# Kernel optimization log

Measured on AMD Instinct MI355X. Metric: run time of the kernel, lower is better.

Reference implementation:

```python
import jax, jax.numpy as jnp
import numpy as np

D_MODEL = 768
D_HEAD = 64
BATCH = 2
SEQ = 4096


def setup_inputs() -> dict:
    key = jax.random.key(0)
    k1, k2, k3, k4, k5 = jax.random.split(key, 5)
    x = jax.random.normal(k1, (BATCH, SEQ, D_MODEL), dtype=jnp.float32)
    # causal mask as the module expects: (seq_len, seq_len) float, 1 where attend allowed
    mask = jnp.tril(jnp.ones((SEQ, SEQ), dtype=jnp.float32))
    # weights initialized like the module: randn / sqrt(d_model)
    scale = 1.0 / np.sqrt(D_MODEL)
    Wq = jax.random.normal(k2, (D_HEAD, D_MODEL), dtype=jnp.float32) * scale
    Wk = jax.random.normal(k3, (D_HEAD, D_MODEL), dtype=jnp.float32) * scale
    Wv = jax.random.normal(k4, (D_HEAD, D_MODEL), dtype=jnp.float32) * scale
    Wo = jax.random.normal(k5, (D_MODEL, D_HEAD), dtype=jnp.float32) * scale
    return {"x": x, "mask": mask, "Wq": Wq, "Wk": Wk, "Wv": Wv, "Wo": Wo}


def reference(x, mask, Wq, Wk, Wv, Wo):
    # q,k,v: (B, S, d_head); Linear with weight (out,in) => x @ W.T
    q = jnp.einsum('bsm,hm->bsh', x, Wq)
    k = jnp.einsum('bsm,hm->bsh', x, Wk)
    v = jnp.einsum('bsm,hm->bsh', x, Wv)
    scores = jnp.einsum('bqd,bkd->bqk', q, k) / np.sqrt(D_HEAD)  # (B,S,S)
    seq_len = x.shape[1]
    m = mask[:seq_len, :seq_len]
    # faithful to the torch code: tril(scores) - 1e10 * (1 - mask)
    scores = jnp.tril(scores) - 1e10 * (1.0 - m)
    attn = jax.nn.softmax(scores, axis=-1)
    z = jnp.einsum('bqk,bkd->bqd', attn, v)  # (B,S,d_head)
    out = jnp.einsum('bsh,mh->bsm', z, Wo)   # (B,S,d_model)
    return out
```

## Files before the change

### kernel.cpp

```cpp
#include <hip/hip_runtime.h>
#include <stdint.h>

#define SEQ 4096
#define DM 768
#define DH 64

typedef __attribute__((ext_vector_type(8))) short short8;
typedef __attribute__((ext_vector_type(4))) short short4v;
typedef __attribute__((ext_vector_type(4))) float f32x4;
typedef __attribute__((ext_vector_type(2))) uint32_t uint2v;

#define LOG2E 1.4426950408889634f

static __device__ __forceinline__ short bf16r(float f) {
  union { float f; uint32_t u; } v; v.f = f;
  uint32_t u = v.u;
  return (short)((u + 0x7FFFu + ((u >> 16) & 1u)) >> 16);
}

static __device__ __forceinline__ float bf16f(uint16_t u) {
  union { uint32_t u; float f; } v; v.u = ((uint32_t)u) << 16;
  return v.f;
}

static __device__ __forceinline__ uint32_t cvtpk(float a, float b) {
  uint32_t r;
  asm("v_cvt_pk_bf16_f32 %0, %1, %2" : "=v"(r) : "v"(a), "v"(b));
  return r;
}

static __device__ __forceinline__ int swz(int row, int b) {
  return row * 128 + (b ^ ((row & 7) << 4));
}

__global__ __launch_bounds__(256) void convert_w(
    const float* __restrict__ Wq, const float* __restrict__ Wk,
    const float* __restrict__ Wv, const float* __restrict__ Wo,
    uint16_t* __restrict__ Wb, uint16_t* __restrict__ Wob) {
  int id = blockIdx.x * 256 + threadIdx.x;
  if (id < 36864) {
    int row = id / 192, c4 = id % 192;
    const float* src = (row < 64) ? (Wq + (size_t)row * DM)
                     : (row < 128) ? (Wk + (size_t)(row - 64) * DM)
                                   : (Wv + (size_t)(row - 128) * DM);
    const float sc = (row < 64) ? (0.125f * LOG2E) : 1.0f;
    float4 v = *(const float4*)(src + c4 * 4);
    short4v pk = { bf16r(v.x * sc), bf16r(v.y * sc), bf16r(v.z * sc), bf16r(v.w * sc) };
    *(short4v*)(Wb + (size_t)row * DM + c4 * 4) = pk;
  } else {
    int t = id - 36864;
    int row = t >> 4, c4 = t & 15;
    float4 v = *(const float4*)(Wo + (size_t)row * DH + c4 * 4);
    short4v pk = { bf16r(v.x), bf16r(v.y), bf16r(v.z), bf16r(v.w) };
    *(short4v*)(Wob + (size_t)row * DH + c4 * 4) = pk;
  }
}

__global__ __launch_bounds__(256) void qkv_proj(
    const float* __restrict__ x, const uint16_t* __restrict__ Wb,
    uint16_t* __restrict__ qg, uint16_t* __restrict__ kg, uint16_t* __restrict__ vg) {
  __shared__ char smem[4096 + 24576] __attribute__((aligned(16)));
  char* Xl = smem;
  char* Wl = smem + 4096;
  const int tid = threadIdx.x;
  const int lane = tid & 63, wv = tid >> 6;
  const int l15 = lane & 15, l4 = lane >> 4;
  const int row0 = blockIdx.x * 32;

  const int xr = tid >> 4, xc4 = tid & 15;
  const int wr0 = tid >> 3, wb16 = tid & 7;
  const int mh = wv & 1, ng = wv >> 1;

  f32x4 acc[6];
  #pragma unroll
  for (int j = 0; j < 6; ++j) acc[j] = (f32x4){0.f, 0.f, 0.f, 0.f};

  float4 xreg[2];
  short8 wreg[6];
  xreg[0] = *(const float4*)(x + (size_t)(row0 + xr) * DM + xc4 * 4);
  xreg[1] = *(const float4*)(x + (size_t)(row0 + 16 + xr) * DM + xc4 * 4);
  #pragma unroll
  for (int i = 0; i < 6; ++i)
    wreg[i] = *(const short8*)(Wb + (size_t)(wr0 + i * 32) * DM + wb16 * 8);

  for (int t = 0; t < 12; ++t) {
    __syncthreads();
    {
      short4v p0 = { bf16r(xreg[0].x), bf16r(xreg[0].y), bf16r(xreg[0].z), bf16r(xreg[0].w) };
      *(short4v*)(Xl + swz(xr, xc4 * 8)) = p0;
      short4v p1 = { bf16r(xreg[1].x), bf16r(xreg[1].y), bf16r(xreg[1].z), bf16r(xreg[1].w) };
      *(short4v*)(Xl + swz(xr + 16, xc4 * 8)) = p1;
    }
    #pragma unroll
    for (int i = 0; i < 6; ++i)
      *(short8*)(Wl + swz(wr0 + i * 32, wb16 * 16)) = wreg[i];
    __syncthreads();
    if (t < 11) {
      const int k0n = (t + 1) * 64;
      xreg[0] = *(const float4*)(x + (size_t)(row0 + xr) * DM + k0n + xc4 * 4);
      xreg[1] = *(const float4*)(x + (size_t)(row0 + 16 + xr) * DM + k0n + xc4 * 4);
      #pragma unroll
      for (int i = 0; i < 6; ++i)
        wreg[i] = *(const short8*)(Wb + (size_t)(wr0 + i * 32) * DM + k0n + wb16 * 8);
    }
    #pragma unroll
    for (int kc = 0; kc < 2; ++kc) {
      short8 af = *(const short8*)(Xl + swz(mh * 16 + l15, kc * 64 + l4 * 16));
      #pragma unroll
      for (int j = 0; j < 6; ++j) {
        int nt = ng * 6 + j;
        short8 bfv = *(const short8*)(Wl + swz(nt * 16 + l15, kc * 64 + l4 * 16));
        acc[j] = __builtin_amdgcn_mfma_f32_16x16x32_bf16(af, bfv, acc[j], 0, 0, 0);
      }
    }
  }
  #pragma unroll
  for (int j = 0; j < 6; ++j) {
    int nt = ng * 6 + j;
    uint16_t* dst = (nt < 4) ? qg : (nt < 8) ? kg : vg;
    int cb = (nt & 3) * 16 + l15;
    #pragma unroll
    for (int r = 0; r < 4; ++r) {
      int row = row0 + mh * 16 + l4 * 4 + r;
      dst[(size_t)row * DH + cb] = (uint16_t)bf16r(acc[j][r]);
    }
  }
}

__global__ __launch_bounds__(256) void attn_split(
    const uint16_t* __restrict__ qg, const uint16_t* __restrict__ kg,
    const uint16_t* __restrict__ vg, uint16_t* __restrict__ zg,
    uint16_t* __restrict__ Opart, float* __restrict__ Ml, int CHUNK, int MAXCH) {
  __shared__ char smem[32768 + 4 * 2048] __attribute__((aligned(16)));

  const int tid = threadIdx.x;
  const int lane = tid & 63, wv = tid >> 6;
  const int l15 = lane & 15, l4 = lane >> 4;
  const int qt = blockIdx.x, ch = blockIdx.y, b = blockIdx.z;
  const int q0 = qt << 6;
  const int kv_lim = q0 + 64;
  const int kv_begin = ch * CHUNK;
  if (kv_begin >= kv_lim) return;
  const int kv_end = min(kv_begin + CHUNK, kv_lim);
  const int ntiles = (kv_end - kv_begin) >> 6;

  const uint16_t* qb = qg + (size_t)b * SEQ * DH;
  const uint16_t* kb = kg + (size_t)b * SEQ * DH;
  const uint16_t* vb = vg + (size_t)b * SEQ * DH;

  const int qrow = q0 + wv * 16 + l15;
  short8 qf0 = *(const short8*)(qb + (size_t)qrow * DH + l4 * 8);
  short8 qf1 = *(const short8*)(qb + (size_t)qrow * DH + 32 + l4 * 8);

  int koffA[4], koffB[4], voffA[4], voffB[4];
  #pragma unroll
  for (int n = 0; n < 4; ++n) {
    koffA[n] = swz(n * 16 + l15, l4 * 16);
    koffB[n] = swz(n * 16 + l15, 64 + l4 * 16);
    int dr = n * 16 + l15;
    voffA[n] = 8192 + dr * 128 + ((l4 * 16) ^ ((dr & 7) << 4));
    voffB[n] = 8192 + dr * 128 + ((64 + l4 * 16) ^ ((dr & 7) << 4));
  }
  int pwoff[4];
  #pragma unroll
  for (int n = 0; n < 4; ++n) pwoff[n] = 32768 + wv * 2048 + swz(l15, n * 32 + l4 * 8);
  const int proff0 = 32768 + wv * 2048 + swz(l15, l4 * 16);
  const int proff1 = 32768 + wv * 2048 + swz(l15, 64 + l4 * 16);

  const int ku = tid - 128;
  const int vg_ = tid >> 3, vdg = tid & 7;
  short8 sreg[4];
  int soff[8];
  if (tid >= 128) {
    #pragma unroll
    for (int i = 0; i < 4; ++i) {
      int c = ku + (i << 7);
      soff[i] = swz(c >> 3, (c & 7) * 16);
    }
  } else {
    #pragma unroll
    for (int j = 0; j < 8; ++j) {
      int d = vdg * 8 + j;
      soff[j] = 8192 + d * 128 + ((vg_ * 8) ^ ((d & 7) << 4));
    }
  }

#define LOAD_REGS(KV0)                                                              \
  if (tid >= 128) {                                                                 \
    _Pragma("unroll")                                                               \
    for (int i = 0; i < 4; ++i) {                                                   \
      int c = ku + (i << 7);                                                        \
      sreg[i] = *(const short8*)(kb + (size_t)((KV0) + (c >> 3)) * DH + (c & 7) * 8); \
    }                                                                               \
  } else {                                                                          \
    _Pragma("unroll")                                                               \
    for (int i = 0; i < 4; ++i)                                                     \
      sreg[i] = *(const short8*)(vb + (size_t)((KV0) + vg_ * 4 + i) * DH + vdg * 8); \
  }

#define STAGE_WRITE(BUF)                                                            \
  {                                                                                 \
    char* base_ = smem + ((BUF) << 14);                                             \
    if (tid >= 128) {                                                               \
      _Pragma("unroll")                                                             \
      for (int i = 0; i < 4; ++i) *(short8*)(base_ + soff[i]) = sreg[i];            \
    } else {                                                                        \
      _Pragma("unroll")                                                             \
      for (int j = 0; j < 8; ++j) {                                                 \
        short4v pk = { sreg[0][j], sreg[1][j], sreg[2][j], sreg[3][j] };            \
        *(short4v*)(base_ + soff[j]) = pk;                                          \
      }                                                                             \
    }                                                                               \
  }

  LOAD_REGS(kv_begin);
  STAGE_WRITE(0);

  f32x4 oaccT[4];
  #pragma unroll
  for (int n = 0; n < 4; ++n) oaccT[n] = (f32x4){0.f, 0.f, 0.f, 0.f};
  float lrun = 0.f;

  for (int T = 0; T < ntiles; ++T) {
    const int kv0 = kv_begin + (T << 6);
    const bool more = (T + 1 < ntiles);
    if (more) { LOAD_REGS(kv0 + 64); }
    __syncthreads();
    char* cb_ = smem + ((T & 1) << 14);

    f32x4 sacc[4];
    #pragma unroll
    for (int n = 0; n < 4; ++n) sacc[n] = (f32x4){0.f, 0.f, 0.f, 0.f};
    __builtin_amdgcn_s_setprio(1);
    #pragma unroll
    for (int n = 0; n < 4; ++n) {
      short8 kf0 = *(const short8*)(cb_ + koffA[n]);
      sacc[n] = __builtin_amdgcn_mfma_f32_16x16x32_bf16(kf0, qf0, sacc[n], 0, 0, 0);
      short8 kf1 = *(const short8*)(cb_ + koffB[n]);
      sacc[n] = __builtin_amdgcn_mfma_f32_16x16x32_bf16(kf1, qf1, sacc[n], 0, 0, 0);
    }
    __builtin_amdgcn_s_setprio(0);

    if (more) { STAGE_WRITE((T + 1) & 1); }

    if (kv0 + 63 > q0) {
      #pragma unroll
      for (int n = 0; n < 4; ++n) {
        #pragma unroll
        for (int r = 0; r < 4; ++r) {
          int kvg = kv0 + n * 16 + l4 * 4 + r;
          if (kvg > qrow) sacc[n][r] = -1e30f;
        }
      }
    }

    float ls = 0.f;
    #pragma unroll
    for (int n = 0; n < 4; ++n) {
      #pragma unroll
      for (int r = 0; r < 4; ++r) {
        float p = __builtin_amdgcn_exp2f(sacc[n][r]);
        sacc[n][r] = p;
        ls += p;
      }
    }
    ls += __shfl_xor(ls, 16);
    ls += __shfl_xor(ls, 32);
    lrun += ls;

    #pragma unroll
    for (int n = 0; n < 4; ++n) {
      uint2v pk = { cvtpk(sacc[n][0], sacc[n][1]), cvtpk(sacc[n][2], sacc[n][3]) };
      *(uint2v*)(smem + pwoff[n]) = pk;
    }
    asm volatile("s_waitcnt lgkmcnt(0)" ::: "memory");
    short8 pa0 = *(const short8*)(smem + proff0);
    short8 pa1 = *(const short8*)(smem + proff1);
    __builtin_amdgcn_s_setprio(1);
    #pragma unroll
    for (int n = 0; n < 4; ++n) {
      short8 vf0 = *(const short8*)(cb_ + voffA[n]);
      oaccT[n] = __builtin_amdgcn_mfma_f32_16x16x32_bf16(vf0, pa0, oaccT[n], 0, 0, 0);
      short8 vf1 = *(const short8*)(cb_ + voffB[n]);
      oaccT[n] = __builtin_amdgcn_mfma_f32_16x16x32_bf16(vf1, pa1, oaccT[n], 0, 0, 0);
    }
    __builtin_amdgcn_s_setprio(0);
  }
#undef LOAD_REGS
#undef STAGE_WRITE

  const int rl = wv * 16 + l15;
  if (MAXCH == 1) {
    float invl = 1.0f / lrun;
    uint16_t* zb = zg + (size_t)b * SEQ * DH;
    #pragma unroll
    for (int n = 0; n < 4; ++n) {
      short4v pk = { bf16r(oaccT[n][0] * invl), bf16r(oaccT[n][1] * invl),
                     bf16r(oaccT[n][2] * invl), bf16r(oaccT[n][3] * invl) };
      *(short4v*)(zb + (size_t)(q0 + rl) * DH + n * 16 + l4 * 4) = pk;
    }
  } else {
    const size_t slot = ((size_t)(b << 6) + qt) * MAXCH + ch;
    uint16_t* op = Opart + slot * 4096;
    #pragma unroll
    for (int n = 0; n < 4; ++n) {
      short4v pk = { bf16r(oaccT[n][0]), bf16r(oaccT[n][1]),
                     bf16r(oaccT[n][2]), bf16r(oaccT[n][3]) };
      *(short4v*)(op + (size_t)rl * 64 + n * 16 + l4 * 4) = pk;
    }
    if (l4 == 0) Ml[slot * 64 + rl] = lrun;
  }
}

__global__ __launch_bounds__(256) void out_proj(
    const uint16_t* __restrict__ Opart, const float* __restrict__ Ml,
    const uint16_t* __restrict__ zg, const uint16_t* __restrict__ Wob,
    float* __restrict__ out, int CHUNK, int MAXCH) {
  __shared__ char smem[4096 + 32768] __attribute__((aligned(16)));
  char* Zl = smem;
  char* Wl = smem + 4096;
  const int tid = threadIdx.x;
  const int lane = tid & 63, wv = tid >> 6;
  const int l15 = lane & 15, l4 = lane >> 4;
  const int row0 = blockIdx.x * 32;
  const int col0 = blockIdx.y * 256;

  {
    const int r = tid >> 3, c0 = (tid & 7) << 3;
    if (MAXCH == 1) {
      short8 v = *(const short8*)(zg + (size_t)(row0 + r) * DH + c0);
      *(short8*)(Zl + swz(r, c0 * 2)) = v;
    } else {
      const int b = row0 >> 12;
      const int rlb = row0 & 4095;
      const int qt = rlb >> 6, q0 = qt << 6;
      const int row_local = (rlb & 63) + r;
      const int nch = (q0 + 64 + CHUNK - 1) / CHUNK;
      const size_t sbase = ((size_t)(b << 6) + qt) * MAXCH;
      float a[8] = {0.f, 0.f, 0.f, 0.f, 0.f, 0.f, 0.f, 0.f};
      float wsum = 0.f;
      for (int ch = 0; ch < nch; ++ch) {
        const size_t s = sbase + ch;
        wsum += Ml[s * 64 + row_local];
        short8 v = *(const short8*)(Opart + s * 4096 + (size_t)row_local * 64 + c0);
        #pragma unroll
        for (int j = 0; j < 8; ++j) a[j] += bf16f((uint16_t)v[j]);
      }
      float inv = 1.0f / wsum;
      short8 pk;
      #pragma unroll
      for (int j = 0; j < 8; ++j) pk[j] = bf16r(a[j] * inv);
      *(short8*)(Zl + swz(r, c0 * 2)) = pk;
    }
  }
  #pragma unroll
  for (int i = 0; i < 8; ++i) {
    int id = tid + (i << 8);
    int m = id >> 3, c8 = id & 7;
    short8 vw = *(const short8*)(Wob + (size_t)(col0 + m) * DH + c8 * 8);
    *(short8*)(Wl + swz(m, c8 * 16)) = vw;
  }
  __syncthreads();

  const int mh = wv & 1, ng = wv >> 1;
  short8 af0 = *(const short8*)(Zl + swz(mh * 16 + l15, l4 * 16));
  short8 af1 = *(const short8*)(Zl + swz(mh * 16 + l15, 64 + l4 * 16));
  f32x4 acc[8];
  #pragma unroll
  for (int j = 0; j < 8; ++j) acc[j] = (f32x4){0.f, 0.f, 0.f, 0.f};
  #pragma unroll
  for (int j = 0; j < 8; ++j) {
    int nt = ng * 8 + j;
    short8 b0 = *(const short8*)(Wl + swz(nt * 16 + l15, l4 * 16));
    acc[j] = __builtin_amdgcn_mfma_f32_16x16x32_bf16(af0, b0, acc[j], 0, 0, 0);
    short8 b1 = *(const short8*)(Wl + swz(nt * 16 + l15, 64 + l4 * 16));
    acc[j] = __builtin_amdgcn_mfma_f32_16x16x32_bf16(af1, b1, acc[j], 0, 0, 0);
  }
  #pragma unroll
  for (int j = 0; j < 8; ++j) {
    int nt = ng * 8 + j;
    #pragma unroll
    for (int r = 0; r < 4; ++r) {
      int row = row0 + mh * 16 + l4 * 4 + r;
      int col = col0 + nt * 16 + l15;
      out[(size_t)row * DM + col] = acc[j][r];
    }
  }
}

extern "C" void kernel_launch(void* const* d_in, const int* in_sizes, int n_in,
                              void* d_out, int out_size, void* d_ws, size_t ws_size,
                              hipStream_t stream) {
  const float* x  = (const float*)d_in[0];
  const float* Wq = (const float*)d_in[2];
  const float* Wk = (const float*)d_in[3];
  const float* Wv = (const float*)d_in[4];
  const float* Wo = (const float*)d_in[5];
  float* out = (float*)d_out;

  const size_t N = (size_t)2 * SEQ * DH;
  uint16_t* qg = (uint16_t*)d_ws;
  uint16_t* kg = qg + N;
  uint16_t* vg = kg + N;
  uint16_t* zg = vg + N;
  uint16_t* Wb = zg + N;
  const size_t WBE = (size_t)192 * DM;
  uint16_t* Wob = Wb + WBE;
  const size_t WOE = (size_t)DM * DH;
  uint16_t* Opart = Wob + WOE;

  int maxch = 16;
  while (maxch > 1) {
    size_t slots = (size_t)2 * 64 * maxch;
    size_t need = 4 * N * 2 + WBE * 2 + WOE * 2 + slots * (4096 * 2 + 64 * 4);
    if (need <= ws_size) break;
    maxch >>= 1;
  }
  const int CHUNK = SEQ / maxch;
  float* Ml = (float*)(Opart + (size_t)2 * 64 * maxch * 4096);

  convert_w<<<192, 256, 0, stream>>>(Wq, Wk, Wv, Wo, Wb, Wob);
  qkv_proj<<<256, 256, 0, stream>>>(x, Wb, qg, kg, vg);
  attn_split<<<dim3(64, maxch, 2), 256, 0, stream>>>(qg, kg, vg, zg, Opart, Ml,
                                                     CHUNK, maxch);
  out_proj<<<dim3(256, 3), 256, 0, stream>>>(Opart, Ml, zg, Wob, out, CHUNK, maxch);
}
```

Measured before the change: 51.32 us.

## Load QKV projection operands directly into registers, dropping LDS staging

The QKV projection kernel no longer stages x and weight tiles through shared memory with barriers. Each wave now loads its MFMA fragments straight from global memory and converts x to bf16 with packed cvt instructions, using 16-row blocks of two waves across 512 blocks. This removes the LDS writes, reads and syncthreads, but each wave re-reads weight rows from global memory or cache, and the loads are strided per lane.

```diff
diff --git a/kernel.cpp b/kernel.cpp
--- a/kernel.cpp
+++ b/kernel.cpp
@@ -27,6 +27,15 @@
   uint32_t r;
   asm("v_cvt_pk_bf16_f32 %0, %1, %2" : "=v"(r) : "v"(a), "v"(b));
   return r;
+}
+
+static __device__ __forceinline__ short8 packA(float4 a0, float4 a1) {
+  union { uint32_t u[4]; short8 s; } r;
+  r.u[0] = cvtpk(a0.x, a0.y);
+  r.u[1] = cvtpk(a0.z, a0.w);
+  r.u[2] = cvtpk(a1.x, a1.y);
+  r.u[3] = cvtpk(a1.z, a1.w);
+  return r.s;
 }
 
 static __device__ __forceinline__ int swz(int row, int b) {
@@ -56,62 +65,32 @@
   }
 }
 
-__global__ __launch_bounds__(256) void qkv_proj(
+__global__ __launch_bounds__(128) void qkv_proj(
     const float* __restrict__ x, const uint16_t* __restrict__ Wb,
     uint16_t* __restrict__ qg, uint16_t* __restrict__ kg, uint16_t* __restrict__ vg) {
-  __shared__ char smem[4096 + 24576] __attribute__((aligned(16)));
-  char* Xl = smem;
-  char* Wl = smem + 4096;
   const int tid = threadIdx.x;
-  const int lane = tid & 63, wv = tid >> 6;
+  const int lane = tid & 63;
+  const int ng = tid >> 6;
   const int l15 = lane & 15, l4 = lane >> 4;
-  const int row0 = blockIdx.x * 32;
-
-  const int xr = tid >> 4, xc4 = tid & 15;
-  const int wr0 = tid >> 3, wb16 = tid & 7;
-  const int mh = wv & 1, ng = wv >> 1;
+  const int rg = blockIdx.x;
+
+  const float* xr_ = x + (size_t)(rg * 16 + l15) * DM + l4 * 8;
+  const uint16_t* wb_ = Wb + (size_t)(ng * 96 + l15) * DM + l4 * 8;
 
   f32x4 acc[6];
   #pragma unroll
   for (int j = 0; j < 6; ++j) acc[j] = (f32x4){0.f, 0.f, 0.f, 0.f};
 
-  float4 xreg[2];
-  short8 wreg[6];
-  xreg[0] = *(const float4*)(x + (size_t)(row0 + xr) * DM + xc4 * 4);
-  xreg[1] = *(const float4*)(x + (size_t)(row0 + 16 + xr) * DM + xc4 * 4);
-  #pragma unroll
-  for (int i = 0; i < 6; ++i)
-    wreg[i] = *(const short8*)(Wb + (size_t)(wr0 + i * 32) * DM + wb16 * 8);
-
-  for (int t = 0; t < 12; ++t) {
-    __syncthreads();
-    {
-      short4v p0 = { bf16r(xreg[0].x), bf16r(xreg[0].y), bf16r(xreg[0].z), bf16r(xreg[0].w) };
-      *(short4v*)(Xl + swz(xr, xc4 * 8)) = p0;
-      short4v p1 = { bf16r(xreg[1].x), bf16r(xreg[1].y), bf16r(xreg[1].z), bf16r(xreg[1].w) };
-      *(short4v*)(Xl + swz(xr + 16, xc4 * 8)) = p1;
-    }
-    #pragma unroll
-    for (int i = 0; i < 6; ++i)
-      *(short8*)(Wl + swz(wr0 + i * 32, wb16 * 16)) = wreg[i];
-    __syncthreads();
-    if (t < 11) {
-      const int k0n = (t + 1) * 64;
-      xreg[0] = *(const float4*)(x + (size_t)(row0 + xr) * DM + k0n + xc4 * 4);
-      xreg[1] = *(const float4*)(x + (size_t)(row0 + 16 + xr) * DM + k0n + xc4 * 4);
-      #pragma unroll
-      for (int i = 0; i < 6; ++i)
-        wreg[i] = *(const short8*)(Wb + (size_t)(wr0 + i * 32) * DM + k0n + wb16 * 8);
-    }
-    #pragma unroll
-    for (int kc = 0; kc < 2; ++kc) {
-      short8 af = *(const short8*)(Xl + swz(mh * 16 + l15, kc * 64 + l4 * 16));
-      #pragma unroll
-      for (int j = 0; j < 6; ++j) {
-        int nt = ng * 6 + j;
-        short8 bfv = *(const short8*)(Wl + swz(nt * 16 + l15, kc * 64 + l4 * 16));
-        acc[j] = __builtin_amdgcn_mfma_f32_16x16x32_bf16(af, bfv, acc[j], 0, 0, 0);
-      }
+  #pragma unroll
+  for (int c = 0; c < 24; ++c) {
+    const int k0 = c * 32;
+    float4 a0 = *(const float4*)(xr_ + k0);
+    float4 a1 = *(const float4*)(xr_ + k0 + 4);
+    short8 af = packA(a0, a1);
+    #pragma unroll
+    for (int j = 0; j < 6; ++j) {
+      short8 bf = *(const short8*)(wb_ + (size_t)j * 16 * DM + k0);
+      acc[j] = __builtin_amdgcn_mfma_f32_16x16x32_bf16(af, bf, acc[j], 0, 0, 0);
     }
   }
   #pragma unroll
@@ -121,7 +100,7 @@
     int cb = (nt & 3) * 16 + l15;
     #pragma unroll
     for (int r = 0; r < 4; ++r) {
-      int row = row0 + mh * 16 + l4 * 4 + r;
+      int row = rg * 16 + l4 * 4 + r;
       dst[(size_t)row * DH + cb] = (uint16_t)bf16r(acc[j][r]);
     }
   }
@@ -420,7 +399,7 @@
   float* Ml = (float*)(Opart + (size_t)2 * 64 * maxch * 4096);
 
   convert_w<<<192, 256, 0, stream>>>(Wq, Wk, Wv, Wo, Wb, Wob);
-  qkv_proj<<<256, 256, 0, stream>>>(x, Wb, qg, kg, vg);
+  qkv_proj<<<512, 128, 0, stream>>>(x, Wb, qg, kg, vg);
   attn_split<<<dim3(64, maxch, 2), 256, 0, stream>>>(qg, kg, vg, zg, Opart, Ml,
                                                      CHUNK, maxch);
   out_proj<<<dim3(256, 3), 256, 0, stream>>>(Opart, Ml, zg, Wob, out, CHUNK, maxch);
```

Result: slower. 62.43 us (+21.7%).
